# Kernel optimization log

Hardware: AMD Instinct MI355X
Metric: run time of the kernel (lower is better)

The kernel has to match this reference:

```python
import jax, jax.numpy as jnp
import numpy as np

NUM_ATOM_TYPE = 120
NUM_BOND_TYPE = 6
NUM_LAYER = 5
EMB_DIM = 300
N_NODES = 50000
N_EDGES = 800000
BN_EPS = 1e-5


def setup_inputs() -> dict:
    key = jax.random.key(0)
    ks = jax.random.split(key, 12)
    x = jax.random.randint(ks[0], (N_NODES, 2), 0, NUM_ATOM_TYPE, dtype=jnp.int32)
    edge_index = jax.random.randint(ks[1], (2, N_EDGES), 0, N_NODES, dtype=jnp.int32)
    edge_attr = jax.random.randint(ks[2], (N_EDGES, 2), 0, 3, dtype=jnp.int32)
    s = 1.0 / np.sqrt(EMB_DIM)
    x_emb = jax.random.uniform(ks[3], (NUM_ATOM_TYPE, EMB_DIM), minval=-s, maxval=s, dtype=jnp.float32)
    edge_emb = jax.random.uniform(ks[4], (NUM_LAYER, NUM_BOND_TYPE, EMB_DIM), minval=-s, maxval=s, dtype=jnp.float32)
    W1 = jax.random.normal(ks[5], (NUM_LAYER, EMB_DIM, 2 * EMB_DIM), dtype=jnp.float32) * s
    b1 = jnp.zeros((NUM_LAYER, 2 * EMB_DIM), dtype=jnp.float32)
    W2 = jax.random.normal(ks[6], (NUM_LAYER, 2 * EMB_DIM, EMB_DIM), dtype=jnp.float32) * (1.0 / np.sqrt(2 * EMB_DIM))
    b2 = jnp.zeros((NUM_LAYER, EMB_DIM), dtype=jnp.float32)
    bn_gamma = jnp.ones((NUM_LAYER, EMB_DIM), dtype=jnp.float32)
    bn_beta = jnp.zeros((NUM_LAYER, EMB_DIM), dtype=jnp.float32)
    return {"x": x, "edge_index": edge_index, "edge_attr": edge_attr,
            "x_emb": x_emb, "edge_emb": edge_emb,
            "W1": W1, "b1": b1, "W2": W2, "b2": b2,
            "bn_gamma": bn_gamma, "bn_beta": bn_beta}


def _forward(x, edge_index, edge_attr, x_emb, edge_emb, W1, b1, W2, b2, bn_gamma, bn_beta):
    n = x.shape[0]
    # node embedding: sum of x_embedding1 over feature columns (faithful to source)
    h = x_emb[x[:, 0]] + x_emb[x[:, 1]]  # [N, D]
    # add self loops once (same for every layer)
    loop = jnp.arange(n, dtype=edge_index.dtype)
    src = jnp.concatenate([edge_index[0], loop])  # [E+N]
    dst = jnp.concatenate([edge_index[1], loop])
    # self-loop edge_attr: zeros with column 0 = 4
    sl = jnp.zeros((n, edge_attr.shape[1]), dtype=edge_attr.dtype).at[:, 0].set(4)
    ea = jnp.concatenate([edge_attr, sl], axis=0)  # [E+N, 2]
    for layer in range(NUM_LAYER):
        # edge embeddings: sum of edge_embedding1 over attr columns (faithful)
        ee = edge_emb[layer][ea[:, 0]] + edge_emb[layer][ea[:, 1]]  # [E+N, D]
        msg = h[src] + ee
        agg = jax.ops.segment_sum(msg, dst, num_segments=n)  # scatter-add
        # GIN MLP (classification branch applies mlp to aggregate only)
        hid = jax.nn.relu(agg @ W1[layer] + b1[layer])
        h = hid @ W2[layer] + b2[layer]
        # BatchNorm1d, training-mode batch statistics
        mu = jnp.mean(h, axis=0)
        var = jnp.var(h, axis=0)
        h = (h - mu) * jax.lax.rsqrt(var + BN_EPS) * bn_gamma[layer] + bn_beta[layer]
        if layer != NUM_LAYER - 1:
            h = jax.nn.relu(h)
        # dropout ratio is 0 -> no-op
    return h  # JK == 'last'


def reference(x, edge_index, edge_attr, x_emb, edge_emb, W1, b1, W2, b2, bn_gamma, bn_beta):
    return _forward(x, edge_index, edge_attr, x_emb, edge_emb, W1, b1, W2, b2, bn_gamma, bn_beta)
```

## Files before the change

kernel.cpp:

```cpp
#include <hip/hip_runtime.h>
#include <hip/hip_bf16.h>

typedef unsigned short u16;
typedef _Float16 f16;
typedef f16 f16x8 __attribute__((ext_vector_type(8)));
typedef f16 half2t __attribute__((ext_vector_type(2)));
typedef u16 u16x8 __attribute__((ext_vector_type(8)));
typedef float f32x4 __attribute__((ext_vector_type(4)));

#define NN 50000
#define NE 800000
#define D  300
#define DP 320
#define HP 640

__device__ __forceinline__ float h2f(u16 u){ f16 h = __builtin_bit_cast(f16, u); return (float)h; }
__device__ __forceinline__ u16 f2h(float f){ f16 h = (f16)f; return __builtin_bit_cast(u16, h); }
__device__ __forceinline__ float hlo(unsigned u){ half2t h = __builtin_bit_cast(half2t, u); return (float)h.x; }
__device__ __forceinline__ float hhi(unsigned u){ half2t h = __builtin_bit_cast(half2t, u); return (float)h.y; }
__device__ __forceinline__ unsigned packh(float x, float y){ half2t h; h.x = (f16)x; h.y = (f16)y; return __builtin_bit_cast(unsigned, h); }

__device__ __forceinline__ void gl_lds16(const void* g, void* l){
  __builtin_amdgcn_global_load_lds((const __attribute__((address_space(1))) unsigned int*)g,
                                   (__attribute__((address_space(3))) unsigned int*)l, 16, 0, 0);
}

__device__ __forceinline__ f32x4 mfma_f16(u16x8 a, u16x8 b, f32x4 c){
  return __builtin_amdgcn_mfma_f32_16x16x32_f16(__builtin_bit_cast(f16x8, a),
                                                __builtin_bit_cast(f16x8, b), c, 0, 0, 0);
}

__global__ void k_count(const int* __restrict__ ei, const int* __restrict__ ea,
                        int* __restrict__ cnt, int* __restrict__ ccnt){
  int e = blockIdx.x * 256 + threadIdx.x;
  if (e < NE){
    int d = ei[NE + e];
    atomicAdd(&cnt[d], 1);
    int t = ea[2*e] * 3 + ea[2*e + 1];
    atomicAdd(&ccnt[d * 12 + t], 1);
  }
}

__global__ void k_scan1(const int* __restrict__ cnt, int* __restrict__ rp, int* __restrict__ bsum){
  __shared__ int s[1024];
  int i = blockIdx.x * 1024 + threadIdx.x;
  int v = (i < NN) ? cnt[i] : 0;
  s[threadIdx.x] = v;
  __syncthreads();
  for (int off = 1; off < 1024; off <<= 1){
    int t = (threadIdx.x >= off) ? s[threadIdx.x - off] : 0;
    __syncthreads();
    s[threadIdx.x] += t;
    __syncthreads();
  }
  if (i < NN) rp[i] = s[threadIdx.x] - v;
  if (threadIdx.x == 1023) bsum[blockIdx.x] = s[1023];
}

__global__ void k_scan2(int* __restrict__ bsum, int nb){
  __shared__ int s[64];
  int v = (threadIdx.x < nb) ? bsum[threadIdx.x] : 0;
  s[threadIdx.x] = v; __syncthreads();
  for (int off = 1; off < 64; off <<= 1){
    int t = (threadIdx.x >= off) ? s[threadIdx.x - off] : 0;
    __syncthreads();
    s[threadIdx.x] += t;
    __syncthreads();
  }
  if (threadIdx.x < nb) bsum[threadIdx.x] = s[threadIdx.x] - v;
}

__global__ void k_scan3(int* __restrict__ rp, int* __restrict__ cur, const int* __restrict__ bsum){
  int i = blockIdx.x * 256 + threadIdx.x;
  if (i < NN){ int v = rp[i] + bsum[i >> 10]; rp[i] = v; cur[i] = v; }
  if (i == 0) rp[NN] = NE;
}

__global__ void k_fill(const int* __restrict__ ei, int* __restrict__ cur, int* __restrict__ pack){
  int e = blockIdx.x * 256 + threadIdx.x;
  if (e >= NE) return;
  int d = ei[NE + e];
  int pos = atomicAdd(&cur[d], 1);
  pack[pos] = ei[e];
}

__global__ void k_wconv(const float* __restrict__ W1, const float* __restrict__ W2,
                        u16* __restrict__ W1t, u16* __restrict__ W2t){
  int i = blockIdx.x * 256 + threadIdx.x;
  {
    int l = i / (HP * DP); int rem = i % (HP * DP); int n = rem / DP, k = rem % DP;
    float v = (n < 600 && k < D) ? W1[((size_t)l * D + k) * 600 + n] : 0.f;
    W1t[i] = f2h(v);
  }
  {
    int l = i / (DP * HP); int rem = i % (DP * HP); int n = rem / HP, k = rem % HP;
    float v = (n < D && k < 600) ? W2[((size_t)l * 600 + k) * D + n] : 0.f;
    W2t[i] = f2h(v);
  }
}

__global__ void k_nodeemb(const int* __restrict__ x, const float* __restrict__ xemb, u16* __restrict__ hb){
  int v = blockIdx.x, c = threadIdx.x;
  float y = 0.f;
  if (c < D){
    int a = x[2*v], b = x[2*v + 1];
    y = xemb[(size_t)a * D + c] + xemb[(size_t)b * D + c];
  }
  hb[(size_t)v * DP + c] = f2h(y);
}

__global__ __launch_bounds__(256) void k_agg(const u16* __restrict__ hb, const int* __restrict__ rp,
    const int* __restrict__ pack, const int* __restrict__ ccnt,
    const float* __restrict__ eemb, u16* __restrict__ agg){
  __shared__ float se[4 * DP];
  for (int i = threadIdx.x; i < 4 * DP; i += 256){
    int t = i / DP, c = i % DP;
    int row = (t == 3) ? 4 : t;
    se[i] = (c < D) ? eemb[row * D + c] : 0.f;
  }
  __syncthreads();
  const int wid = threadIdx.x >> 6, lane = threadIdx.x & 63;
  const int v = blockIdx.x * 4 + wid;
  if (v >= NN) return;
  const char* __restrict__ hbb = (const char*)hb;
  const unsigned lo8 = (unsigned)lane * 8u;
  const unsigned lo4 = 512u + (unsigned)lane * 4u;
  float a0, a1, a2, a3, a4 = 0.f, a5 = 0.f;
  {
    unsigned off = (unsigned)v * 640u;
    uint2 u = *(const uint2*)(hbb + off + lo8);
    a0 = hlo(u.x); a1 = hhi(u.x); a2 = hlo(u.y); a3 = hhi(u.y);
    if (lane < 32){ unsigned uw = *(const unsigned*)(hbb + off + lo4); a4 = hlo(uw); a5 = hhi(uw); }
  }
  int p = rp[v];
  const int pe = rp[v + 1];
  for (; p + 2 <= pe; p += 2){
    unsigned off0 = (unsigned)pack[p] * 640u;
    unsigned off1 = (unsigned)pack[p + 1] * 640u;
    uint2 u0 = *(const uint2*)(hbb + off0 + lo8);
    uint2 u1 = *(const uint2*)(hbb + off1 + lo8);
    unsigned w0v = 0, w1v = 0;
    if (lane < 32){
      w0v = *(const unsigned*)(hbb + off0 + lo4);
      w1v = *(const unsigned*)(hbb + off1 + lo4);
    }
    a0 += hlo(u0.x) + hlo(u1.x);
    a1 += hhi(u0.x) + hhi(u1.x);
    a2 += hlo(u0.y) + hlo(u1.y);
    a3 += hhi(u0.y) + hhi(u1.y);
    a4 += hlo(w0v) + hlo(w1v);
    a5 += hhi(w0v) + hhi(w1v);
  }
  if (p < pe){
    unsigned off0 = (unsigned)pack[p] * 640u;
    uint2 u0 = *(const uint2*)(hbb + off0 + lo8);
    a0 += hlo(u0.x); a1 += hhi(u0.x); a2 += hlo(u0.y); a3 += hhi(u0.y);
    if (lane < 32){ unsigned w0v = *(const unsigned*)(hbb + off0 + lo4); a4 += hlo(w0v); a5 += hhi(w0v); }
  }
  const int* cc = ccnt + (size_t)v * 12;
  int4 cA = *(const int4*)cc;
  int4 cB = *(const int4*)(cc + 4);
  int c8 = cc[8];
  float w0f = (float)(2 * cA.x + cA.y + cA.z + cA.w + cB.z + 1);
  float w1f = (float)(cA.y + cA.w + 2 * cB.x + cB.y + cB.w);
  float w2f = (float)(cA.z + cB.y + cB.z + cB.w + 2 * c8);
  {
    const float4 e0v = *(const float4*)&se[0 * DP + 4 * lane];
    const float4 e1v = *(const float4*)&se[1 * DP + 4 * lane];
    const float4 e2v = *(const float4*)&se[2 * DP + 4 * lane];
    const float4 e4v = *(const float4*)&se[3 * DP + 4 * lane];
    a0 += w0f * e0v.x + w1f * e1v.x + w2f * e2v.x + e4v.x;
    a1 += w0f * e0v.y + w1f * e1v.y + w2f * e2v.y + e4v.y;
    a2 += w0f * e0v.z + w1f * e1v.z + w2f * e2v.z + e4v.z;
    a3 += w0f * e0v.w + w1f * e1v.w + w2f * e2v.w + e4v.w;
  }
  char* ab = (char*)agg;
  unsigned oo = (unsigned)v * 640u;
  uint2 st; st.x = packh(a0, a1); st.y = packh(a2, a3);
  *(uint2*)(ab + oo + lo8) = st;
  if (lane < 32){
    int cI = 256 + 2 * lane;
    a4 += w0f * se[0 * DP + cI]     + w1f * se[1 * DP + cI]     + w2f * se[2 * DP + cI]     + se[3 * DP + cI];
    a5 += w0f * se[0 * DP + cI + 1] + w1f * se[1 * DP + cI + 1] + w2f * se[2 * DP + cI + 1] + se[3 * DP + cI + 1];
    *(unsigned*)(ab + oo + lo4) = packh(a4, a5);
  }
}

template<int KPAD, bool RELU, int OUTM>
__global__ __launch_bounds__(256) void k_gemm(const u16* __restrict__ A, const u16* __restrict__ Bt,
    const float* __restrict__ bias, int bias_n,
    void* __restrict__ C, int ldc, int ccols, int M, int Nrows,
    float* __restrict__ sums){
  __shared__ __attribute__((aligned(16))) u16 lA[128 * 32];
  __shared__ __attribute__((aligned(16))) u16 lB[128 * 32];
  const int tid = threadIdx.x;
  const int lane = tid & 63;
  const int wid = tid >> 6;
  const int gm0 = blockIdx.x * 128, gn0 = blockIdx.y * 128;
  const int wr = (wid >> 1) * 64, wc = (wid & 1) * 64;
  int ar1 = gm0 + (tid >> 2);       if (ar1 >= M) ar1 = M - 1;
  int ar2 = gm0 + 64 + (tid >> 2);  if (ar2 >= M) ar2 = M - 1;
  int br1 = gn0 + (tid >> 2);       if (br1 >= Nrows) br1 = Nrows - 1;
  int br2 = gn0 + 64 + (tid >> 2);  if (br2 >= Nrows) br2 = Nrows - 1;
  const int kb = (tid & 3) * 8;
  const int wbase = (tid & ~63) * 8;
  f32x4 acc[4][4] = {};
  for (int k0 = 0; k0 < KPAD; k0 += 32){
    __syncthreads();
    gl_lds16(A  + (size_t)ar1 * KPAD + k0 + kb, lA + wbase);
    gl_lds16(A  + (size_t)ar2 * KPAD + k0 + kb, lA + wbase + 2048);
    gl_lds16(Bt + (size_t)br1 * KPAD + k0 + kb, lB + wbase);
    gl_lds16(Bt + (size_t)br2 * KPAD + k0 + kb, lB + wbase + 2048);
    asm volatile("s_waitcnt vmcnt(0)" ::: "memory");
    __syncthreads();
    u16x8 af[4], bfr[4];
    #pragma unroll
    for (int m = 0; m < 4; ++m) af[m]  = *(const u16x8*)&lA[(wr + m * 16 + (lane & 15)) * 32 + (lane >> 4) * 8];
    #pragma unroll
    for (int n = 0; n < 4; ++n) bfr[n] = *(const u16x8*)&lB[(wc + n * 16 + (lane & 15)) * 32 + (lane >> 4) * 8];
    #pragma unroll
    for (int m = 0; m < 4; ++m)
      #pragma unroll
      for (int n = 0; n < 4; ++n)
        acc[m][n] = mfma_f16(af[m], bfr[n], acc[m][n]);
  }
  float sn[4] = {0.f, 0.f, 0.f, 0.f}, qn[4] = {0.f, 0.f, 0.f, 0.f};
  #pragma unroll
  for (int m = 0; m < 4; ++m){
    const int row0 = gm0 + wr + m * 16 + (lane >> 4) * 4;
    #pragma unroll
    for (int n = 0; n < 4; ++n){
      const int col = gn0 + wc + n * 16 + (lane & 15);
      if (col >= ccols) continue;
      const float bv = (col < bias_n) ? bias[col] : 0.f;
      #pragma unroll
      for (int r = 0; r < 4; ++r){
        const int row = row0 + r;
        if (row < M){
          float vv = acc[m][n][r] + bv;
          if (RELU) vv = fmaxf(vv, 0.f);
          if (OUTM == 0){
            ((float*)C)[(size_t)row * ldc + col] = vv;
            sn[n] += vv; qn[n] += vv * vv;
          } else {
            ((u16*)C)[(size_t)row * ldc + col] = f2h(vv);
          }
        }
      }
    }
  }
  if (OUTM == 0){
    #pragma unroll
    for (int n = 0; n < 4; ++n){
      const int col = gn0 + wc + n * 16 + (lane & 15);
      float s = sn[n], q = qn[n];
      s += __shfl_xor(s, 16); q += __shfl_xor(q, 16);
      s += __shfl_xor(s, 32); q += __shfl_xor(q, 32);
      if (col < ccols && (lane >> 4) == 0){
        atomicAdd(&sums[col], s);
        atomicAdd(&sums[DP + col], q);
      }
    }
  }
}

template<bool LAST>
__global__ void k_bnapply(const float* h2, const float* __restrict__ sums,
    const float* __restrict__ gamma, const float* __restrict__ beta,
    u16* __restrict__ hb, float* outp){
  int r = blockIdx.x, c = threadIdx.x;
  float y = 0.f;
  if (c < D){
    float mu  = sums[c] * (1.f / NN);
    float var = sums[DP + c] * (1.f / NN) - mu * mu;
    float x = h2[(size_t)r * D + c];
    float s = var + 1e-5f;
    float inv = rsqrtf(s);
    inv = inv * (1.5f - 0.5f * s * inv * inv);
    y = (x - mu) * inv * gamma[c] + beta[c];
    if (!LAST) y = fmaxf(y, 0.f);
  }
  if (LAST){ if (c < D) outp[(size_t)r * D + c] = y; }
  else hb[(size_t)r * DP + c] = f2h(y);
}

extern "C" void kernel_launch(void* const* d_in, const int* in_sizes, int n_in,
                              void* d_out, int out_size, void* d_ws, size_t ws_size,
                              hipStream_t stream){
  (void)in_sizes; (void)n_in; (void)out_size; (void)ws_size;
  const int*   x    = (const int*)d_in[0];
  const int*   ei   = (const int*)d_in[1];
  const int*   ea   = (const int*)d_in[2];
  const float* xemb = (const float*)d_in[3];
  const float* eemb = (const float*)d_in[4];
  const float* W1   = (const float*)d_in[5];
  const float* b1   = (const float*)d_in[6];
  const float* W2   = (const float*)d_in[7];
  const float* b2   = (const float*)d_in[8];
  const float* gam  = (const float*)d_in[9];
  const float* bet  = (const float*)d_in[10];
  float* out = (float*)d_out;

  char* w = (char*)d_ws;
  size_t off = 0;
  auto alloc = [&](size_t b){ void* p = w + off; off += (b + 255) & ~(size_t)255; return p; };
  u16* hid   = (u16*)alloc((size_t)NN * HP * 2);
  u16* hb    = hid;
  u16* aggb  = (u16*)alloc((size_t)NN * DP * 2);
  u16* W1t   = (u16*)alloc((size_t)5 * HP * DP * 2);
  u16* W2t   = (u16*)alloc((size_t)5 * DP * HP * 2);
  int* rp    = (int*)alloc((NN + 1) * 4);
  int* cnt   = (int*)alloc((size_t)NN * 4);
  int* cur   = (int*)alloc((size_t)NN * 4);
  int* bsum  = (int*)alloc(64 * 4);
  int* pack  = (int*)alloc((size_t)NE * 4);
  int* ccnt  = (int*)alloc((size_t)NN * 12 * 4);
  float* sums= (float*)alloc(2 * DP * 4);
  float* h2  = out;

  hipMemsetAsync(cnt, 0, NN * 4, stream);
  hipMemsetAsync(ccnt, 0, (size_t)NN * 12 * 4, stream);
  k_count<<<NE / 256, 256, 0, stream>>>(ei, ea, cnt, ccnt);
  k_scan1<<<(NN + 1023) / 1024, 1024, 0, stream>>>(cnt, rp, bsum);
  k_scan2<<<1, 64, 0, stream>>>(bsum, (NN + 1023) / 1024);
  k_scan3<<<(NN + 255) / 256, 256, 0, stream>>>(rp, cur, bsum);
  k_fill<<<NE / 256, 256, 0, stream>>>(ei, cur, pack);
  k_wconv<<<(5 * HP * DP) / 256, 256, 0, stream>>>(W1, W2, W1t, W2t);
  k_nodeemb<<<NN, DP, 0, stream>>>(x, xemb, hb);

  for (int l = 0; l < 5; ++l){
    k_agg<<<(NN + 3) / 4, 256, 0, stream>>>(hb, rp, pack, ccnt, eemb + (size_t)l * 6 * D, aggb);
    k_gemm<DP, true, 1><<<dim3((NN + 127) / 128, HP / 128), 256, 0, stream>>>(
        aggb, W1t + (size_t)l * HP * DP, b1 + l * 600, 600, hid, HP, HP, NN, HP, nullptr);
    hipMemsetAsync(sums, 0, 2 * DP * 4, stream);
    k_gemm<HP, false, 0><<<dim3((NN + 127) / 128, 3), 256, 0, stream>>>(
        hid, W2t + (size_t)l * DP * HP, b2 + l * D, D, h2, D, D, NN, DP, sums);
    if (l < 4) k_bnapply<false><<<NN, DP, 0, stream>>>(h2, sums, gam + l * D, bet + l * D, hb, nullptr);
    else       k_bnapply<true ><<<NN, DP, 0, stream>>>(h2, sums, gam + l * D, bet + l * D, nullptr, out);
  }
}
```

Measured before the change: 1.536 ms.

## Fuse the two MLP GEMMs into one kernel, keeping the hidden tile in LDS

Replaces the two separate GEMM launches with a single k_mlp kernel. Each 512-thread block computes a 64-row tile of the hidden layer, stores it in an XOR-swizzled LDS buffer, then runs the second GEMM from LDS, so the 50000x640 fp16 hidden tensor is never written to or read back from global memory. Operands are loaded straight from global memory into registers instead of being staged through LDS with global_load_lds, which gives up the shared reuse of weight tiles across waves. Buffers are padded to 50048 rows so out-of-range A rows can be read without clamping.

```diff
diff --git a/kernel.cpp b/kernel.cpp
--- a/kernel.cpp
+++ b/kernel.cpp
@@ -13,17 +13,14 @@
 #define D  300
 #define DP 320
 #define HP 640
+#define MT 64
+#define NROWPAD 50048
 
 __device__ __forceinline__ float h2f(u16 u){ f16 h = __builtin_bit_cast(f16, u); return (float)h; }
 __device__ __forceinline__ u16 f2h(float f){ f16 h = (f16)f; return __builtin_bit_cast(u16, h); }
 __device__ __forceinline__ float hlo(unsigned u){ half2t h = __builtin_bit_cast(half2t, u); return (float)h.x; }
 __device__ __forceinline__ float hhi(unsigned u){ half2t h = __builtin_bit_cast(half2t, u); return (float)h.y; }
 __device__ __forceinline__ unsigned packh(float x, float y){ half2t h; h.x = (f16)x; h.y = (f16)y; return __builtin_bit_cast(unsigned, h); }
-
-__device__ __forceinline__ void gl_lds16(const void* g, void* l){
-  __builtin_amdgcn_global_load_lds((const __attribute__((address_space(1))) unsigned int*)g,
-                                   (__attribute__((address_space(3))) unsigned int*)l, 16, 0, 0);
-}
 
 __device__ __forceinline__ f32x4 mfma_f16(u16x8 a, u16x8 b, f32x4 c){
   return __builtin_amdgcn_mfma_f32_16x16x32_f16(__builtin_bit_cast(f16x8, a),
@@ -186,80 +183,111 @@
   }
 }
 
-template<int KPAD, bool RELU, int OUTM>
-__global__ __launch_bounds__(256) void k_gemm(const u16* __restrict__ A, const u16* __restrict__ Bt,
-    const float* __restrict__ bias, int bias_n,
-    void* __restrict__ C, int ldc, int ccols, int M, int Nrows,
-    float* __restrict__ sums){
-  __shared__ __attribute__((aligned(16))) u16 lA[128 * 32];
-  __shared__ __attribute__((aligned(16))) u16 lB[128 * 32];
+__global__ __launch_bounds__(512, 4) void k_mlp(const u16* __restrict__ agg,
+    const u16* __restrict__ W1t, const u16* __restrict__ W2t,
+    const float* __restrict__ b1, const float* __restrict__ b2,
+    float* __restrict__ h2, float* __restrict__ sums){
+  __shared__ __attribute__((aligned(16))) u16 hid[MT * HP];
   const int tid = threadIdx.x;
-  const int lane = tid & 63;
-  const int wid = tid >> 6;
-  const int gm0 = blockIdx.x * 128, gn0 = blockIdx.y * 128;
-  const int wr = (wid >> 1) * 64, wc = (wid & 1) * 64;
-  int ar1 = gm0 + (tid >> 2);       if (ar1 >= M) ar1 = M - 1;
-  int ar2 = gm0 + 64 + (tid >> 2);  if (ar2 >= M) ar2 = M - 1;
-  int br1 = gn0 + (tid >> 2);       if (br1 >= Nrows) br1 = Nrows - 1;
-  int br2 = gn0 + 64 + (tid >> 2);  if (br2 >= Nrows) br2 = Nrows - 1;
-  const int kb = (tid & 3) * 8;
-  const int wbase = (tid & ~63) * 8;
-  f32x4 acc[4][4] = {};
-  for (int k0 = 0; k0 < KPAD; k0 += 32){
-    __syncthreads();
-    gl_lds16(A  + (size_t)ar1 * KPAD + k0 + kb, lA + wbase);
-    gl_lds16(A  + (size_t)ar2 * KPAD + k0 + kb, lA + wbase + 2048);
-    gl_lds16(Bt + (size_t)br1 * KPAD + k0 + kb, lB + wbase);
-    gl_lds16(Bt + (size_t)br2 * KPAD + k0 + kb, lB + wbase + 2048);
-    asm volatile("s_waitcnt vmcnt(0)" ::: "memory");
-    __syncthreads();
-    u16x8 af[4], bfr[4];
-    #pragma unroll
-    for (int m = 0; m < 4; ++m) af[m]  = *(const u16x8*)&lA[(wr + m * 16 + (lane & 15)) * 32 + (lane >> 4) * 8];
-    #pragma unroll
-    for (int n = 0; n < 4; ++n) bfr[n] = *(const u16x8*)&lB[(wc + n * 16 + (lane & 15)) * 32 + (lane >> 4) * 8];
-    #pragma unroll
-    for (int m = 0; m < 4; ++m)
-      #pragma unroll
-      for (int n = 0; n < 4; ++n)
-        acc[m][n] = mfma_f16(af[m], bfr[n], acc[m][n]);
-  }
-  float sn[4] = {0.f, 0.f, 0.f, 0.f}, qn[4] = {0.f, 0.f, 0.f, 0.f};
+  const int lane = tid & 63, w = tid >> 6;
+  const int mh = w >> 2, nq = w & 3;
+  const int r0 = blockIdx.x * MT;
+  const unsigned l15 = (unsigned)(lane & 15);
+  const unsigned kb16 = ((unsigned)(lane >> 4)) * 16u;
+  const char* aggB = (const char*)agg;
+  const char* w1B  = (const char*)W1t;
+  const char* w2B  = (const char*)W2t;
+
+  const unsigned arow0 = (unsigned)(r0 + mh * 32) + l15;
   #pragma unroll
-  for (int m = 0; m < 4; ++m){
-    const int row0 = gm0 + wr + m * 16 + (lane >> 4) * 4;
-    #pragma unroll
-    for (int n = 0; n < 4; ++n){
-      const int col = gn0 + wc + n * 16 + (lane & 15);
-      if (col >= ccols) continue;
-      const float bv = (col < bias_n) ? bias[col] : 0.f;
+  for (int pass = 0; pass < 2; ++pass){
+    const int nbase = nq * 160 + pass * 80;
+    f32x4 acc[2][5] = {};
+    #pragma unroll
+    for (int ks = 0; ks < 10; ++ks){
+      u16x8 af[2], bf[5];
+      #pragma unroll
+      for (int m = 0; m < 2; ++m)
+        af[m] = *(const u16x8*)(aggB + (size_t)(arow0 + m * 16) * 640 + ks * 64 + kb16);
+      #pragma unroll
+      for (int n = 0; n < 5; ++n){
+        unsigned col = (unsigned)(nbase + n * 16) + l15;
+        bf[n] = *(const u16x8*)(w1B + (size_t)col * 640 + ks * 64 + kb16);
+      }
+      #pragma unroll
+      for (int m = 0; m < 2; ++m)
+        #pragma unroll
+        for (int n = 0; n < 5; ++n)
+          acc[m][n] = mfma_f16(af[m], bf[n], acc[m][n]);
+    }
+    #pragma unroll
+    for (int m = 0; m < 2; ++m){
+      #pragma unroll
+      for (int n = 0; n < 5; ++n){
+        const int col = nbase + n * 16 + (int)l15;
+        const float bv = (col < 600) ? b1[col] : 0.f;
+        #pragma unroll
+        for (int r = 0; r < 4; ++r){
+          const unsigned row = (unsigned)(mh * 32 + m * 16) + ((unsigned)(lane >> 4)) * 4u + (unsigned)r;
+          const float vv = fmaxf(acc[m][n][r] + bv, 0.f);
+          const unsigned byte = row * 1280u + ((2u * (unsigned)col) ^ ((row & 7u) << 4));
+          *(u16*)((char*)hid + byte) = f2h(vv);
+        }
+      }
+    }
+  }
+  __syncthreads();
+
+  f32x4 acc[2][5] = {};
+  #pragma unroll
+  for (int ks = 0; ks < 20; ++ks){
+    u16x8 af[2], bf[5];
+    #pragma unroll
+    for (int m = 0; m < 2; ++m){
+      const unsigned row = (unsigned)(mh * 32 + m * 16) + l15;
+      const unsigned byte = row * 1280u + (((unsigned)ks * 64u + kb16) ^ ((row & 7u) << 4));
+      af[m] = *(const u16x8*)((const char*)hid + byte);
+    }
+    #pragma unroll
+    for (int n = 0; n < 5; ++n){
+      const unsigned col = (unsigned)(nq * 80 + n * 16) + l15;
+      bf[n] = *(const u16x8*)(w2B + (size_t)col * 1280 + ks * 64 + kb16);
+    }
+    #pragma unroll
+    for (int m = 0; m < 2; ++m)
+      #pragma unroll
+      for (int n = 0; n < 5; ++n)
+        acc[m][n] = mfma_f16(af[m], bf[n], acc[m][n]);
+  }
+  float sn[5] = {0,0,0,0,0}, qn[5] = {0,0,0,0,0};
+  #pragma unroll
+  for (int m = 0; m < 2; ++m){
+    const int row0 = r0 + mh * 32 + m * 16 + (lane >> 4) * 4;
+    #pragma unroll
+    for (int n = 0; n < 5; ++n){
+      const int col = nq * 80 + n * 16 + (int)l15;
+      if (col >= D) continue;
+      const float bv = b2[col];
       #pragma unroll
       for (int r = 0; r < 4; ++r){
         const int row = row0 + r;
-        if (row < M){
-          float vv = acc[m][n][r] + bv;
-          if (RELU) vv = fmaxf(vv, 0.f);
-          if (OUTM == 0){
-            ((float*)C)[(size_t)row * ldc + col] = vv;
-            sn[n] += vv; qn[n] += vv * vv;
-          } else {
-            ((u16*)C)[(size_t)row * ldc + col] = f2h(vv);
-          }
+        if (row < NN){
+          const float vv = acc[m][n][r] + bv;
+          h2[(size_t)row * D + col] = vv;
+          sn[n] += vv; qn[n] += vv * vv;
         }
       }
     }
   }
-  if (OUTM == 0){
-    #pragma unroll
-    for (int n = 0; n < 4; ++n){
-      const int col = gn0 + wc + n * 16 + (lane & 15);
-      float s = sn[n], q = qn[n];
-      s += __shfl_xor(s, 16); q += __shfl_xor(q, 16);
-      s += __shfl_xor(s, 32); q += __shfl_xor(q, 32);
-      if (col < ccols && (lane >> 4) == 0){
-        atomicAdd(&sums[col], s);
-        atomicAdd(&sums[DP + col], q);
-      }
+  #pragma unroll
+  for (int n = 0; n < 5; ++n){
+    const int col = nq * 80 + n * 16 + (int)l15;
+    float s = sn[n], q = qn[n];
+    s += __shfl_xor(s, 16); q += __shfl_xor(q, 16);
+    s += __shfl_xor(s, 32); q += __shfl_xor(q, 32);
+    if (col < D && (lane >> 4) == 0){
+      atomicAdd(&sums[col], s);
+      atomicAdd(&sums[DP + col], q);
     }
   }
 }
@@ -304,9 +332,8 @@
   char* w = (char*)d_ws;
   size_t off = 0;
   auto alloc = [&](size_t b){ void* p = w + off; off += (b + 255) & ~(size_t)255; return p; };
-  u16* hid   = (u16*)alloc((size_t)NN * HP * 2);
-  u16* hb    = hid;
-  u16* aggb  = (u16*)alloc((size_t)NN * DP * 2);
+  u16* hb    = (u16*)alloc((size_t)NROWPAD * DP * 2);
+  u16* aggb  = (u16*)alloc((size_t)NROWPAD * DP * 2);
   u16* W1t   = (u16*)alloc((size_t)5 * HP * DP * 2);
   u16* W2t   = (u16*)alloc((size_t)5 * DP * HP * 2);
   int* rp    = (int*)alloc((NN + 1) * 4);
@@ -330,11 +357,10 @@
 
   for (int l = 0; l < 5; ++l){
     k_agg<<<(NN + 3) / 4, 256, 0, stream>>>(hb, rp, pack, ccnt, eemb + (size_t)l * 6 * D, aggb);
-    k_gemm<DP, true, 1><<<dim3((NN + 127) / 128, HP / 128), 256, 0, stream>>>(
-        aggb, W1t + (size_t)l * HP * DP, b1 + l * 600, 600, hid, HP, HP, NN, HP, nullptr);
     hipMemsetAsync(sums, 0, 2 * DP * 4, stream);
-    k_gemm<HP, false, 0><<<dim3((NN + 127) / 128, 3), 256, 0, stream>>>(
-        hid, W2t + (size_t)l * DP * HP, b2 + l * D, D, h2, D, D, NN, DP, sums);
+    k_mlp<<<NROWPAD / MT, 512, 0, stream>>>(aggb,
+        W1t + (size_t)l * HP * DP, W2t + (size_t)l * DP * HP,
+        b1 + l * 600, b2 + l * D, h2, sums);
     if (l < 4) k_bnapply<false><<<NN, DP, 0, stream>>>(h2, sums, gam + l * D, bet + l * D, hb, nullptr);
     else       k_bnapply<true ><<<NN, DP, 0, stream>>>(h2, sums, gam + l * D, bet + l * D, nullptr, out);
   }
```

Result: slower. 2.005 ms (+30.6%).
